# Optimization experiments

Hardware: AMD Instinct MI355X
Metric: run time of the kernel (lower is better)

## Reference

```python
import jax, jax.numpy as jnp
import numpy as np

T, B, D, H, L = 512, 64, 512, 512, 2  # seq_len, batch, input, hidden, layers (bidirectional)


def _xavier(k, shape):
    fan_out, fan_in = shape
    lim = np.sqrt(6.0 / (fan_in + fan_out)).astype(np.float32)
    return jax.random.uniform(k, shape, minval=-lim, maxval=lim, dtype=jnp.float32)


def setup_inputs() -> dict:
    key = jax.random.key(0)
    ks = jax.random.split(key, 1 + 4 * L)
    inp = {"x": jax.random.normal(ks[0], (T, B, D), dtype=jnp.float32)}
    idx = 1
    for layer in range(L):
        din = D if layer == 0 else 2 * H
        for d in ("f", "b"):
            inp[f"w_ih{layer}_{d}"] = _xavier(ks[idx], (4 * H, din)); idx += 1
            inp[f"w_hh{layer}_{d}"] = _xavier(ks[idx], (4 * H, H)); idx += 1
            # xavier_uniform() in the module fills both biases with forget_bias=1.0
            inp[f"b_ih{layer}_{d}"] = jnp.ones((4 * H,), jnp.float32)
            inp[f"b_hh{layer}_{d}"] = jnp.ones((4 * H,), jnp.float32)
    return inp


def _lstm_dir(x, w_ih, w_hh, b_ih, b_hh, reverse):
    """Run one direction of a VarLSTMCell over time. x: [T,B,Din] -> h: [T,B,H]."""
    hdim = w_hh.shape[1]
    # precompute input contribution for all timesteps (same math as per-step matmul)
    xg = jnp.einsum('tbd,gd->tbg', x, w_ih) + b_ih + b_hh  # [T,B,4H]

    def step(carry, xg_t):
        h, c = carry
        gates = xg_t + h @ w_hh.T  # [B,4H]
        i, f, g, o = jnp.split(gates, 4, axis=-1)  # PyTorch LSTMCell gate order
        c = jax.nn.sigmoid(f) * c + jax.nn.sigmoid(i) * jnp.tanh(g)
        h = jax.nn.sigmoid(o) * jnp.tanh(c)
        return (h, c), h

    init = (jnp.zeros((x.shape[1], hdim), x.dtype), jnp.zeros((x.shape[1], hdim), x.dtype))
    _, hs = jax.lax.scan(step, init, xg, reverse=reverse)
    return hs  # [T,B,H], time-ordered (scan reverse keeps original ordering)


def reference(x,
              w_ih0_f, w_hh0_f, b_ih0_f, b_hh0_f,
              w_ih0_b, w_hh0_b, b_ih0_b, b_hh0_b,
              w_ih1_f, w_hh1_f, b_ih1_f, b_hh1_f,
              w_ih1_b, w_hh1_b, b_ih1_b, b_hh1_b):
    params = [
        ((w_ih0_f, w_hh0_f, b_ih0_f, b_hh0_f), (w_ih0_b, w_hh0_b, b_ih0_b, b_hh0_b)),
        ((w_ih1_f, w_hh1_f, b_ih1_f, b_hh1_f), (w_ih1_b, w_hh1_b, b_ih1_b, b_hh1_b)),
    ]
    out = x
    for fwd_p, bwd_p in params:
        h_f = _lstm_dir(out, *fwd_p, reverse=False)
        h_b = _lstm_dir(out, *bwd_p, reverse=True)
        out = jnp.concatenate([h_f, h_b], axis=-1)  # [T,B,2H]
        # dropout=0.0 -> inter-layer dropout is identity
    return out
```

## Files before the change

kernel.cpp:

```cpp
#include <hip/hip_runtime.h>
#include <hip/hip_bf16.h>
#include <stdint.h>


typedef __attribute__((ext_vector_type(8))) _Float16 half8;
typedef __attribute__((ext_vector_type(4))) float f32x4;
typedef unsigned long long ull;

#define AL(p) __hip_atomic_load((p), __ATOMIC_RELAXED, __HIP_MEMORY_SCOPE_AGENT)
#define AS(p, v) __hip_atomic_store((p), (v), __ATOMIC_RELAXED, __HIP_MEMORY_SCOPE_AGENT)

#define TAGMASK 0x4000400040004000ULL
#define PAT_L1A 0x0000400000004000ULL
#define PAT_L1B 0x4000000040000000ULL
#define PAT_INIT_LO 0x40004000u
#define PAT_INIT_HI 0x00000000u

__device__ __forceinline__ unsigned short f2h(float f) {
    union { _Float16 h; unsigned short u; } c; c.h = (_Float16)f; return c.u;
}
__device__ __forceinline__ float h2f(unsigned short u) {
    union { _Float16 h; unsigned short u; } c; c.u = u; return (float)c.h;
}

__global__ __launch_bounds__(256) void prep_kernel(
    const float* __restrict__ x,
    const float* __restrict__ w0f, const float* __restrict__ w0b,
    const float* __restrict__ w1f, const float* __restrict__ w1b,
    const float* __restrict__ bi0f, const float* __restrict__ bh0f,
    const float* __restrict__ bi0b, const float* __restrict__ bh0b,
    const float* __restrict__ bi1f, const float* __restrict__ bh1f,
    const float* __restrict__ bi1b, const float* __restrict__ bh1b,
    unsigned short* __restrict__ xh,
    unsigned short* __restrict__ wihh,
    float* __restrict__ bias,
    uint32_t* __restrict__ hbufi)
{
    const long total = 5801984L;
    long stride = (long)gridDim.x * blockDim.x;
    for (long i = (long)blockIdx.x * blockDim.x + threadIdx.x; i < total; i += stride) {
        if (i < 4194304L) {
            float4 v = ((const float4*)x)[i];
            ushort4 o; o.x=f2h(v.x); o.y=f2h(v.y); o.z=f2h(v.z); o.w=f2h(v.w);
            ((ushort4*)xh)[i] = o;
        } else if (i < 5767168L) {
            long j = i - 4194304L;
            const float* src; long sq;
            if (j < 262144L)       { src = w0f; sq = j;            }
            else if (j < 524288L)  { src = w0b; sq = j - 262144L;  }
            else if (j < 1048576L) { src = w1f; sq = j - 524288L;  }
            else                   { src = w1b; sq = j - 1048576L; }
            float4 v = ((const float4*)src)[sq];
            ushort4 o; o.x=f2h(v.x); o.y=f2h(v.y); o.z=f2h(v.z); o.w=f2h(v.w);
            ((ushort4*)wihh)[j] = o;
        } else if (i < 5769216L) {
            long j = i - 5767168L;
            int ld = (int)(j >> 9);
            long cq = j & 511L;
            const float* bi = ld==0?bi0f: ld==1?bi0b: ld==2?bi1f:bi1b;
            const float* bh = ld==0?bh0f: ld==1?bh0b: ld==2?bh1f:bh1b;
            float4 a = ((const float4*)bi)[cq];
            float4 b = ((const float4*)bh)[cq];
            float4 o; o.x=a.x+b.x; o.y=a.y+b.y; o.z=a.z+b.z; o.w=a.w+b.w;
            ((float4*)bias)[ld*512 + cq] = o;
        } else {
            long j = i - 5769216L;
            uint4 p; p.x=PAT_INIT_LO; p.y=PAT_INIT_HI; p.z=PAT_INIT_LO; p.w=PAT_INIT_HI;
            ((uint4*)hbufi)[j] = p;
        }
    }
}

__global__ __launch_bounds__(256) void gemm_xg(
    const unsigned short* __restrict__ A,
    const unsigned short* __restrict__ Wf,
    const unsigned short* __restrict__ Wb,
    unsigned short* __restrict__ xg,
    int Din)
{
    __shared__ __align__(16) unsigned short As[4096];
    __shared__ __align__(16) unsigned short Bs[4096];
    const int dir = blockIdx.z;
    const unsigned short* W = dir ? Wb : Wf;
    unsigned short* out = xg + (size_t)dir * 32768 * 2048;
    const int bn = blockIdx.x, bm = blockIdx.y;
    const int tid = threadIdx.x;
    const int wave = tid >> 6, lane = tid & 63;
    const int q = lane >> 4, ln = lane & 15;
    const int wm = wave >> 1, wn = wave & 1;

    f32x4 acc[4][4];
#pragma unroll
    for (int a = 0; a < 4; ++a)
#pragma unroll
        for (int b = 0; b < 4; ++b) acc[a][b] = (f32x4){0.f, 0.f, 0.f, 0.f};

    const int kiter = Din >> 5;
    for (int kb = 0; kb < kiter; ++kb) {
        __syncthreads();
#pragma unroll
        for (int i = 0; i < 2; ++i) {
            int off = i*4096 + wave*1024 + lane*16;
            int row = off >> 6;
            int kel = (off & 63) >> 1;
            const unsigned short* sa = A + (size_t)(bm*128 + row)*Din + kb*32 + kel;
            const unsigned short* sb = W + (size_t)(bn*128 + row)*Din + kb*32 + kel;
            __builtin_amdgcn_global_load_lds(
                (const __attribute__((address_space(1))) uint32_t*)sa,
                (__attribute__((address_space(3))) uint32_t*)((char*)As + i*4096 + wave*1024),
                16, 0, 0);
            __builtin_amdgcn_global_load_lds(
                (const __attribute__((address_space(1))) uint32_t*)sb,
                (__attribute__((address_space(3))) uint32_t*)((char*)Bs + i*4096 + wave*1024),
                16, 0, 0);
        }
        __syncthreads();
        half8 af[4], bf[4];
#pragma unroll
        for (int mt = 0; mt < 4; ++mt)
            af[mt] = *(const half8*)((const char*)As + (wm*64 + mt*16 + ln)*64 + q*16);
#pragma unroll
        for (int nt = 0; nt < 4; ++nt)
            bf[nt] = *(const half8*)((const char*)Bs + (wn*64 + nt*16 + ln)*64 + q*16);
#pragma unroll
        for (int mt = 0; mt < 4; ++mt)
#pragma unroll
            for (int nt = 0; nt < 4; ++nt)
                acc[mt][nt] = __builtin_amdgcn_mfma_f32_16x16x32_f16(af[mt], bf[nt], acc[mt][nt], 0, 0, 0);
    }
    const int tt = bm*2 + wm;
#pragma unroll
    for (int mt = 0; mt < 4; ++mt)
#pragma unroll
        for (int nt = 0; nt < 4; ++nt) {
            int col = bn*128 + wn*64 + nt*16 + ln;
            int gate = col >> 9, colg = col & 511;
            union { unsigned short u[4]; ull v; } p;
#pragma unroll
            for (int r = 0; r < 4; ++r) p.u[r] = f2h(acc[mt][nt][r]);
            __builtin_nontemporal_store(p.v,
                (ull*)(out + (((size_t)tt*4 + gate)*512 + colg)*64 + mt*16 + q*4));
        }
}

__global__ __launch_bounds__(64) void rec_kernel(
    const unsigned short* __restrict__ xg,
    const float* __restrict__ whhf,
    const float* __restrict__ whhb,
    const float* __restrict__ bias,
    unsigned short* __restrict__ hbuf,
    unsigned short* __restrict__ outh,
    float* __restrict__ outf,
    const int layer)
{
    __shared__ __align__(16) unsigned short whh[32768];
    __shared__ __align__(16) unsigned short htile[256];
    const int bx = blockIdx.x;
    const int dir = bx & 1, g = (bx >> 1) & 31, bh = bx >> 6;
    const int lane = threadIdx.x;
    const int q = lane >> 4, ln = lane & 15;
    const float* whhg = dir ? whhb : whhf;
    const ull pat0 = layer ? PAT_L1A : 0ULL;
    const ull pat1 = layer ? PAT_L1B : TAGMASK;

    {
        const int kkw = lane >> 2, qqw = lane & 3;
#pragma unroll 4
        for (int Lr = 0; Lr < 64; ++Lr) {
            int gate = Lr >> 4, r16 = Lr & 15;
            const float* src = whhg + (size_t)(gate*512 + g*16 + r16) * 512 + lane*8;
            float4 v0 = *(const float4*)src;
            float4 v1 = *(const float4*)(src + 4);
            union { unsigned short u[8]; half8 v; } p;
            p.u[0]=f2h(v0.x); p.u[1]=f2h(v0.y); p.u[2]=f2h(v0.z); p.u[3]=f2h(v0.w);
            p.u[4]=f2h(v1.x); p.u[5]=f2h(v1.y); p.u[6]=f2h(v1.z); p.u[7]=f2h(v1.w);
            *(half8*)((char*)whh + gate*16384 + kkw*1024 + qqw*256 + r16*16) = p.v;
        }
    }
    __syncthreads();

    const unsigned short* xgd = xg + (size_t)dir * 32768 * 2048;
    const float* biasd = bias + dir * 2048;
    float bv0 = biasd[0*512 + g*16 + ln];
    float bv1 = biasd[1*512 + g*16 + ln];
    float bv2 = biasd[2*512 + g*16 + ln];
    float bv3 = biasd[3*512 + g*16 + ln];

    float carr[4] = {0.f, 0.f, 0.f, 0.f};

#pragma unroll 1
    for (int s = 0; s < 512; ++s) {
        const int t = dir ? (511 - s) : s;

        ull xv64[4];
#pragma unroll
        for (int nt = 0; nt < 4; ++nt)
            xv64[nt] = __builtin_nontemporal_load(
                (const ull*)(xgd + ((size_t)(t*4 + nt)*512 + g*16 + ln)*64 + bh*16 + q*4));

        f32x4 a0 = {0,0,0,0}, a1 = {0,0,0,0}, a2 = {0,0,0,0}, a3 = {0,0,0,0};

        if (s > 0) {
            const int slot_r = (s - 1) & 3;
            const ull epat = (((s - 1) >> 2) & 1) ? pat1 : pat0;
            const ull* hb = (const ull*)(hbuf
                + ((size_t)(slot_r*2 + dir)*64 + bh*16 + ln)*512) + q*2;
            ull hv[32];
#pragma unroll
            for (int kk = 0; kk < 16; ++kk) {
                hv[2*kk]   = AL(hb + kk*8);
                hv[2*kk+1] = AL(hb + kk*8 + 1);
            }
            for (int it = 0; it < (1 << 13); ++it) {
                unsigned stale = 0;
#pragma unroll
                for (int c = 0; c < 32; ++c)
                    stale |= ((hv[c] & TAGMASK) != epat) ? (1u << c) : 0u;
                if (!stale) break;
#pragma unroll
                for (int c = 0; c < 32; ++c)
                    if (stale & (1u << c))
                        hv[c] = AL(hb + (c >> 1)*8 + (c & 1));
            }
#pragma unroll
            for (int kk = 0; kk < 16; ++kk) {
                union { ull u[2]; half8 v; } af;
                af.u[0] = hv[2*kk]   & ~TAGMASK;
                af.u[1] = hv[2*kk+1] & ~TAGMASK;
                const char* wb = (const char*)whh + kk*1024 + lane*16;
                half8 b0 = *(const half8*)(wb);
                half8 b1 = *(const half8*)(wb + 16384);
                half8 b2 = *(const half8*)(wb + 32768);
                half8 b3 = *(const half8*)(wb + 49152);
                a0 = __builtin_amdgcn_mfma_f32_16x16x32_f16(af.v, b0, a0, 0, 0, 0);
                a1 = __builtin_amdgcn_mfma_f32_16x16x32_f16(af.v, b1, a1, 0, 0, 0);
                a2 = __builtin_amdgcn_mfma_f32_16x16x32_f16(af.v, b2, a2, 0, 0, 0);
                a3 = __builtin_amdgcn_mfma_f32_16x16x32_f16(af.v, b3, a3, 0, 0, 0);
            }
        }

        unsigned short hs[4];
#pragma unroll
        for (int r = 0; r < 4; ++r) {
            float gi = a0[r] + h2f((unsigned short)(xv64[0] >> (16*r))) + bv0;
            float gf = a1[r] + h2f((unsigned short)(xv64[1] >> (16*r))) + bv1;
            float gg = a2[r] + h2f((unsigned short)(xv64[2] >> (16*r))) + bv2;
            float go = a3[r] + h2f((unsigned short)(xv64[3] >> (16*r))) + bv3;
            float si = 1.f / (1.f + __expf(-gi));
            float sf = 1.f / (1.f + __expf(-gf));
            float so = 1.f / (1.f + __expf(-go));
            float tg = 2.f / (1.f + __expf(-2.f*gg)) - 1.f;
            float c  = sf * carr[r] + si * tg;
            carr[r] = c;
            float th = 2.f / (1.f + __expf(-2.f*c)) - 1.f;
            hs[r] = f2h(so * th);
        }

#pragma unroll
        for (int r = 0; r < 4; ++r) htile[(q*4 + r)*16 + ln] = hs[r];
        __syncthreads();
        ull hv64 = *(const ull*)(htile + (lane >> 2)*16 + (lane & 3)*4);
        const int row  = bh*16 + (lane >> 2);
        const int colw = g*16 + (lane & 3)*4;

        const int slot_w = s & 3;
        const ull wpat = ((s >> 2) & 1) ? pat1 : pat0;
        AS((ull*)(hbuf + ((size_t)(slot_w*2 + dir)*64 + row)*512 + colw), hv64 | wpat);

        if (layer == 0) {
            __builtin_nontemporal_store(hv64,
                (ull*)(outh + ((size_t)t*64 + row)*1024 + dir*512 + colw));
        } else {
            union { ull u; unsigned short us[4]; } pu; pu.u = hv64;
            union { ull u; float f[2]; } o0, o1;
            o0.f[0] = h2f(pu.us[0]); o0.f[1] = h2f(pu.us[1]);
            o1.f[0] = h2f(pu.us[2]); o1.f[1] = h2f(pu.us[3]);
            ull* dst = (ull*)(outf + ((size_t)t*64 + row)*1024 + dir*512 + colw);
            __builtin_nontemporal_store(o0.u, dst);
            __builtin_nontemporal_store(o1.u, dst + 1);
        }
        __syncthreads();
    }
}

extern "C" void kernel_launch(void* const* d_in, const int* in_sizes, int n_in,
                              void* d_out, int out_size, void* d_ws, size_t ws_size,
                              hipStream_t stream)
{
    (void)in_sizes; (void)n_in; (void)out_size; (void)ws_size;
    const float* x       = (const float*)d_in[0];
    const float* w_ih0_f = (const float*)d_in[1];
    const float* w_hh0_f = (const float*)d_in[2];
    const float* b_ih0_f = (const float*)d_in[3];
    const float* b_hh0_f = (const float*)d_in[4];
    const float* w_ih0_b = (const float*)d_in[5];
    const float* w_hh0_b = (const float*)d_in[6];
    const float* b_ih0_b = (const float*)d_in[7];
    const float* b_hh0_b = (const float*)d_in[8];
    const float* w_ih1_f = (const float*)d_in[9];
    const float* w_hh1_f = (const float*)d_in[10];
    const float* b_ih1_f = (const float*)d_in[11];
    const float* b_hh1_f = (const float*)d_in[12];
    const float* w_ih1_b = (const float*)d_in[13];
    const float* w_hh1_b = (const float*)d_in[14];
    const float* b_ih1_b = (const float*)d_in[15];
    const float* b_hh1_b = (const float*)d_in[16];

    char* ws = (char*)d_ws;
    unsigned short* xg    = (unsigned short*)(ws + 0);
    unsigned short* wihh  = (unsigned short*)(ws + 268435456L);
    float*          bias  = (float*)         (ws + 281018368L);
    unsigned short* hbuf  = (unsigned short*)(ws + 281051136L);

    unsigned short* in1 = (unsigned short*)d_out;
    unsigned short* xh  = (unsigned short*)((char*)d_out + 67108864L);
    float* outf = (float*)d_out;

    prep_kernel<<<dim3(1024), dim3(256), 0, stream>>>(
        x, w_ih0_f, w_ih0_b, w_ih1_f, w_ih1_b,
        b_ih0_f, b_hh0_f, b_ih0_b, b_hh0_b,
        b_ih1_f, b_hh1_f, b_ih1_b, b_hh1_b,
        xh, wihh, bias, (uint32_t*)hbuf);

    gemm_xg<<<dim3(16, 256, 2), dim3(256), 0, stream>>>(
        xh, wihh, wihh + 1048576, xg, 512);
    rec_kernel<<<dim3(256), dim3(64), 0, stream>>>(
        xg, w_hh0_f, w_hh0_b, bias, hbuf, in1, (float*)nullptr, 0);

    gemm_xg<<<dim3(16, 256, 2), dim3(256), 0, stream>>>(
        in1, wihh + 2097152, wihh + 4194304, xg, 1024);
    rec_kernel<<<dim3(256), dim3(64), 0, stream>>>(
        xg, w_hh1_f, w_hh1_b, bias + 4096, hbuf,
        (unsigned short*)nullptr, outf, 1);
}
```

Before: 6.215 ms.

## Restructure recurrent kernel: 8-wave blocks, register-resident weights, cooperative h staging

The recurrent kernel moves from 256 single-wave blocks to 128 blocks of 512 threads. Each wave now holds its slice of W_hh in registers instead of LDS and computes one gate for 16 columns. The block loads the previous hidden tile cooperatively with cache-bypassing dwordx4 loads and spin-checks tag bits, then stages it in swizzled LDS. Partial gate sums are exchanged through LDS, and only two waves run the nonlinearity and write h. This cuts redundant per-wave polling of the global h buffer and the LDS weight traffic, at the cost of extra block barriers per step and fewer blocks.

```diff
diff --git a/kernel.cpp b/kernel.cpp
--- a/kernel.cpp
+++ b/kernel.cpp
@@ -5,12 +5,13 @@
 
 typedef __attribute__((ext_vector_type(8))) _Float16 half8;
 typedef __attribute__((ext_vector_type(4))) float f32x4;
+typedef __attribute__((ext_vector_type(4))) uint32_t u32x4;
 typedef unsigned long long ull;
 
-#define AL(p) __hip_atomic_load((p), __ATOMIC_RELAXED, __HIP_MEMORY_SCOPE_AGENT)
 #define AS(p, v) __hip_atomic_store((p), (v), __ATOMIC_RELAXED, __HIP_MEMORY_SCOPE_AGENT)
 
 #define TAGMASK 0x4000400040004000ULL
+#define TM32    0x40004000u
 #define PAT_L1A 0x0000400000004000ULL
 #define PAT_L1B 0x4000000040000000ULL
 #define PAT_INIT_LO 0x40004000u
@@ -143,7 +144,7 @@
         }
 }
 
-__global__ __launch_bounds__(64) void rec_kernel(
+__global__ __launch_bounds__(512, 2) void rec_kernel(
     const unsigned short* __restrict__ xg,
     const float* __restrict__ whhf,
     const float* __restrict__ whhb,
@@ -153,133 +154,153 @@
     float* __restrict__ outf,
     const int layer)
 {
-    __shared__ __align__(16) unsigned short whh[32768];
-    __shared__ __align__(16) unsigned short htile[256];
+    __shared__ __align__(16) unsigned short h_lds[8192];
+    __shared__ __align__(16) float accbuf[2048];
+    __shared__ __align__(16) unsigned short htile[512];
+
     const int bx = blockIdx.x;
-    const int dir = bx & 1, g = (bx >> 1) & 31, bh = bx >> 6;
-    const int lane = threadIdx.x;
-    const int q = lane >> 4, ln = lane & 15;
+    const int dir = bx & 1, bh = (bx >> 1) & 3, cg = bx >> 3;
+    const int R0 = bh * 16, C0 = cg * 32;
+    const int tid = threadIdx.x;
+    const int wv = tid >> 6, lane = tid & 63;
+    const int g = wv >> 1, wc = wv & 1;
+    const int ln = lane & 15, q = lane >> 4;
     const float* whhg = dir ? whhb : whhf;
+
     const ull pat0 = layer ? PAT_L1A : 0ULL;
     const ull pat1 = layer ? PAT_L1B : TAGMASK;
-
+    const uint32_t ep0 = (uint32_t)(pat0 & 0xffffffffULL);
+    const uint32_t ep1 = (uint32_t)(pat1 & 0xffffffffULL);
+
+    half8 wreg[16];
     {
-        const int kkw = lane >> 2, qqw = lane & 3;
-#pragma unroll 4
-        for (int Lr = 0; Lr < 64; ++Lr) {
-            int gate = Lr >> 4, r16 = Lr & 15;
-            const float* src = whhg + (size_t)(gate*512 + g*16 + r16) * 512 + lane*8;
-            float4 v0 = *(const float4*)src;
-            float4 v1 = *(const float4*)(src + 4);
+        const int wrow = g*512 + C0 + wc*16 + ln;
+        const float* wsrc = whhg + (size_t)wrow * 512 + q*8;
+#pragma unroll
+        for (int kk = 0; kk < 16; ++kk) {
+            float4 v0 = *(const float4*)(wsrc + kk*32);
+            float4 v1 = *(const float4*)(wsrc + kk*32 + 4);
             union { unsigned short u[8]; half8 v; } p;
             p.u[0]=f2h(v0.x); p.u[1]=f2h(v0.y); p.u[2]=f2h(v0.z); p.u[3]=f2h(v0.w);
             p.u[4]=f2h(v1.x); p.u[5]=f2h(v1.y); p.u[6]=f2h(v1.z); p.u[7]=f2h(v1.w);
-            *(half8*)((char*)whh + gate*16384 + kkw*1024 + qqw*256 + r16*16) = p.v;
+            wreg[kk] = p.v;
         }
     }
-    __syncthreads();
 
     const unsigned short* xgd = xg + (size_t)dir * 32768 * 2048;
     const float* biasd = bias + dir * 2048;
-    float bv0 = biasd[0*512 + g*16 + ln];
-    float bv1 = biasd[1*512 + g*16 + ln];
-    float bv2 = biasd[2*512 + g*16 + ln];
-    float bv3 = biasd[3*512 + g*16 + ln];
-
+    const int myc = C0 + wc*16 + ln;
+    float bv0 = biasd[0*512 + myc];
+    float bv1 = biasd[1*512 + myc];
+    float bv2 = biasd[2*512 + myc];
+    float bv3 = biasd[3*512 + myc];
     float carr[4] = {0.f, 0.f, 0.f, 0.f};
+
+    const int prow = tid >> 5;
+    const int pcol = (tid & 31) * 16;
+    const int swz  = (prow & 7) << 4;
+    const int wb0 = prow*1024 + ((pcol*2)      ^ swz);
+    const int wb1 = prow*1024 + ((pcol*2 + 16) ^ swz);
 
 #pragma unroll 1
     for (int s = 0; s < 512; ++s) {
         const int t = dir ? (511 - s) : s;
 
-        ull xv64[4];
-#pragma unroll
-        for (int nt = 0; nt < 4; ++nt)
-            xv64[nt] = __builtin_nontemporal_load(
-                (const ull*)(xgd + ((size_t)(t*4 + nt)*512 + g*16 + ln)*64 + bh*16 + q*4));
-
-        f32x4 a0 = {0,0,0,0}, a1 = {0,0,0,0}, a2 = {0,0,0,0}, a3 = {0,0,0,0};
+        ull xv64[4] = {0,0,0,0};
+        if (g == 0) {
+#pragma unroll
+            for (int nt_ = 0; nt_ < 4; ++nt_)
+                xv64[nt_] = __builtin_nontemporal_load(
+                    (const ull*)(xgd + ((size_t)(t*4 + nt_)*512 + myc)*64 + bh*16 + q*4));
+        }
 
         if (s > 0) {
             const int slot_r = (s - 1) & 3;
-            const ull epat = (((s - 1) >> 2) & 1) ? pat1 : pat0;
-            const ull* hb = (const ull*)(hbuf
-                + ((size_t)(slot_r*2 + dir)*64 + bh*16 + ln)*512) + q*2;
-            ull hv[32];
+            const uint32_t ep = (((s - 1) >> 2) & 1) ? ep1 : ep0;
+            const uint32_t* src = (const uint32_t*)(hbuf
+                + ((size_t)(slot_r*2 + dir)*64 + R0 + prow)*512 + pcol);
+            u32x4 r0, r1;
+            bool ok = false;
+            for (int it = 0; it < (1 << 13) && !ok; ++it) {
+                asm volatile(
+                    "global_load_dwordx4 %0, %2, off sc0 sc1\n\t"
+                    "global_load_dwordx4 %1, %3, off sc0 sc1\n\t"
+                    "s_waitcnt vmcnt(0)"
+                    : "=&v"(r0), "=&v"(r1)
+                    : "v"(src), "v"(src + 4)
+                    : "memory");
+                uint32_t bad = 0;
+#pragma unroll
+                for (int c = 0; c < 4; ++c) bad |= (r0[c] ^ ep) & TM32;
+#pragma unroll
+                for (int c = 0; c < 4; ++c) bad |= (r1[c] ^ ep) & TM32;
+                ok = (bad == 0);
+            }
+#pragma unroll
+            for (int c = 0; c < 4; ++c) { r0[c] &= ~TM32; r1[c] &= ~TM32; }
+            *(u32x4*)((char*)h_lds + wb0) = r0;
+            *(u32x4*)((char*)h_lds + wb1) = r1;
+        }
+        __syncthreads();
+
+        f32x4 acc = (f32x4){0.f, 0.f, 0.f, 0.f};
+        if (s > 0) {
+            const char* hbase = (const char*)h_lds + ln*1024;
+            const int lswz = (ln & 7) << 4;
 #pragma unroll
             for (int kk = 0; kk < 16; ++kk) {
-                hv[2*kk]   = AL(hb + kk*8);
-                hv[2*kk+1] = AL(hb + kk*8 + 1);
+                half8 a = *(const half8*)(hbase + ((kk*64 + q*16) ^ lswz));
+                acc = __builtin_amdgcn_mfma_f32_16x16x32_f16(a, wreg[kk], acc, 0, 0, 0);
             }
-            for (int it = 0; it < (1 << 13); ++it) {
-                unsigned stale = 0;
-#pragma unroll
-                for (int c = 0; c < 32; ++c)
-                    stale |= ((hv[c] & TAGMASK) != epat) ? (1u << c) : 0u;
-                if (!stale) break;
-#pragma unroll
-                for (int c = 0; c < 32; ++c)
-                    if (stale & (1u << c))
-                        hv[c] = AL(hb + (c >> 1)*8 + (c & 1));
+        }
+        *(f32x4*)&accbuf[(wv*16 + ln)*16 + q*4] = acc;
+        __syncthreads();
+
+        if (g == 0) {
+            f32x4 a0 = *(const f32x4*)&accbuf[((0*2 + wc)*16 + ln)*16 + q*4];
+            f32x4 a1 = *(const f32x4*)&accbuf[((1*2 + wc)*16 + ln)*16 + q*4];
+            f32x4 a2 = *(const f32x4*)&accbuf[((2*2 + wc)*16 + ln)*16 + q*4];
+            f32x4 a3 = *(const f32x4*)&accbuf[((3*2 + wc)*16 + ln)*16 + q*4];
+            unsigned short hs[4];
+#pragma unroll
+            for (int r = 0; r < 4; ++r) {
+                float gi = a0[r] + h2f((unsigned short)(xv64[0] >> (16*r))) + bv0;
+                float gf = a1[r] + h2f((unsigned short)(xv64[1] >> (16*r))) + bv1;
+                float gg = a2[r] + h2f((unsigned short)(xv64[2] >> (16*r))) + bv2;
+                float go = a3[r] + h2f((unsigned short)(xv64[3] >> (16*r))) + bv3;
+                float si = 1.f / (1.f + __expf(-gi));
+                float sf = 1.f / (1.f + __expf(-gf));
+                float so = 1.f / (1.f + __expf(-go));
+                float tg = 2.f / (1.f + __expf(-2.f*gg)) - 1.f;
+                float c  = sf * carr[r] + si * tg;
+                carr[r] = c;
+                float th = 2.f / (1.f + __expf(-2.f*c)) - 1.f;
+                hs[r] = f2h(so * th);
             }
-#pragma unroll
-            for (int kk = 0; kk < 16; ++kk) {
-                union { ull u[2]; half8 v; } af;
-                af.u[0] = hv[2*kk]   & ~TAGMASK;
-                af.u[1] = hv[2*kk+1] & ~TAGMASK;
-                const char* wb = (const char*)whh + kk*1024 + lane*16;
-                half8 b0 = *(const half8*)(wb);
-                half8 b1 = *(const half8*)(wb + 16384);
-                half8 b2 = *(const half8*)(wb + 32768);
-                half8 b3 = *(const half8*)(wb + 49152);
-                a0 = __builtin_amdgcn_mfma_f32_16x16x32_f16(af.v, b0, a0, 0, 0, 0);
-                a1 = __builtin_amdgcn_mfma_f32_16x16x32_f16(af.v, b1, a1, 0, 0, 0);
-                a2 = __builtin_amdgcn_mfma_f32_16x16x32_f16(af.v, b2, a2, 0, 0, 0);
-                a3 = __builtin_amdgcn_mfma_f32_16x16x32_f16(af.v, b3, a3, 0, 0, 0);
+            unsigned short* ht = htile + wc*256;
+#pragma unroll
+            for (int r = 0; r < 4; ++r) ht[(q*4 + r)*16 + ln] = hs[r];
+            ull hv64 = *(const ull*)(ht + (lane >> 2)*16 + (lane & 3)*4);
+            const int row  = R0 + (lane >> 2);
+            const int colw = C0 + wc*16 + (lane & 3)*4;
+
+            const int slot_w = s & 3;
+            const ull wpat = ((s >> 2) & 1) ? pat1 : pat0;
+            AS((ull*)(hbuf + ((size_t)(slot_w*2 + dir)*64 + row)*512 + colw), hv64 | wpat);
+
+            if (layer == 0) {
+                __builtin_nontemporal_store(hv64,
+                    (ull*)(outh + ((size_t)t*64 + row)*1024 + dir*512 + colw));
+            } else {
+                union { ull u; unsigned short us[4]; } pu; pu.u = hv64;
+                union { ull u; float f[2]; } o0, o1;
+                o0.f[0] = h2f(pu.us[0]); o0.f[1] = h2f(pu.us[1]);
+                o1.f[0] = h2f(pu.us[2]); o1.f[1] = h2f(pu.us[3]);
+                ull* dst = (ull*)(outf + ((size_t)t*64 + row)*1024 + dir*512 + colw);
+                __builtin_nontemporal_store(o0.u, dst);
+                __builtin_nontemporal_store(o1.u, dst + 1);
             }
         }
-
-        unsigned short hs[4];
-#pragma unroll
-        for (int r = 0; r < 4; ++r) {
-            float gi = a0[r] + h2f((unsigned short)(xv64[0] >> (16*r))) + bv0;
-            float gf = a1[r] + h2f((unsigned short)(xv64[1] >> (16*r))) + bv1;
-            float gg = a2[r] + h2f((unsigned short)(xv64[2] >> (16*r))) + bv2;
-            float go = a3[r] + h2f((unsigned short)(xv64[3] >> (16*r))) + bv3;
-            float si = 1.f / (1.f + __expf(-gi));
-            float sf = 1.f / (1.f + __expf(-gf));
-            float so = 1.f / (1.f + __expf(-go));
-            float tg = 2.f / (1.f + __expf(-2.f*gg)) - 1.f;
-            float c  = sf * carr[r] + si * tg;
-            carr[r] = c;
-            float th = 2.f / (1.f + __expf(-2.f*c)) - 1.f;
-            hs[r] = f2h(so * th);
-        }
-
-#pragma unroll
-        for (int r = 0; r < 4; ++r) htile[(q*4 + r)*16 + ln] = hs[r];
-        __syncthreads();
-        ull hv64 = *(const ull*)(htile + (lane >> 2)*16 + (lane & 3)*4);
-        const int row  = bh*16 + (lane >> 2);
-        const int colw = g*16 + (lane & 3)*4;
-
-        const int slot_w = s & 3;
-        const ull wpat = ((s >> 2) & 1) ? pat1 : pat0;
-        AS((ull*)(hbuf + ((size_t)(slot_w*2 + dir)*64 + row)*512 + colw), hv64 | wpat);
-
-        if (layer == 0) {
-            __builtin_nontemporal_store(hv64,
-                (ull*)(outh + ((size_t)t*64 + row)*1024 + dir*512 + colw));
-        } else {
-            union { ull u; unsigned short us[4]; } pu; pu.u = hv64;
-            union { ull u; float f[2]; } o0, o1;
-            o0.f[0] = h2f(pu.us[0]); o0.f[1] = h2f(pu.us[1]);
-            o1.f[0] = h2f(pu.us[2]); o1.f[1] = h2f(pu.us[3]);
-            ull* dst = (ull*)(outf + ((size_t)t*64 + row)*1024 + dir*512 + colw);
-            __builtin_nontemporal_store(o0.u, dst);
-            __builtin_nontemporal_store(o1.u, dst + 1);
-        }
-        __syncthreads();
     }
 }
 
@@ -324,12 +345,12 @@
 
     gemm_xg<<<dim3(16, 256, 2), dim3(256), 0, stream>>>(
         xh, wihh, wihh + 1048576, xg, 512);
-    rec_kernel<<<dim3(256), dim3(64), 0, stream>>>(
+    rec_kernel<<<dim3(128), dim3(512), 0, stream>>>(
         xg, w_hh0_f, w_hh0_b, bias, hbuf, in1, (float*)nullptr, 0);
 
     gemm_xg<<<dim3(16, 256, 2), dim3(256), 0, stream>>>(
         in1, wihh + 2097152, wihh + 4194304, xg, 1024);
-    rec_kernel<<<dim3(256), dim3(64), 0, stream>>>(
+    rec_kernel<<<dim3(128), dim3(512), 0, stream>>>(
         xg, w_hh1_f, w_hh1_b, bias + 4096, hbuf,
         (unsigned short*)nullptr, outf, 1);
 }
```

Result: faster. 5.589 ms (-10.1%).

## Interleave both directions per block with register-resident weights and pipelined h loads

Applied to the files above, without the earlier changes.

Restructures the recurrent kernel so each 64-thread block handles both forward and backward directions for 4 hidden columns across all four gates. W_hh slices are held in registers instead of LDS, and the h ring is read with inline-asm dwordx4 coherent loads. Loads for one direction are issued while the other direction computes, hiding the cross-block polling latency. Gate values are regrouped with lane shuffles instead of an LDS tile and barriers, and each lane publishes a single tagged fp16 value. The grid doubles to 512 blocks with launch_bounds(64,2). The trade-offs are heavy register pressure, hand-written vmcnt waits that must match the exact count of loads in flight, and a new per-element tag scheme that must stay consistent with the hbuf initialisation.

```diff
diff --git a/kernel.cpp b/kernel.cpp
--- a/kernel.cpp
+++ b/kernel.cpp
@@ -5,14 +5,11 @@
 
 typedef __attribute__((ext_vector_type(8))) _Float16 half8;
 typedef __attribute__((ext_vector_type(4))) float f32x4;
+typedef __attribute__((ext_vector_type(4))) uint32_t u32x4;
 typedef unsigned long long ull;
 
-#define AL(p) __hip_atomic_load((p), __ATOMIC_RELAXED, __HIP_MEMORY_SCOPE_AGENT)
-#define AS(p, v) __hip_atomic_store((p), (v), __ATOMIC_RELAXED, __HIP_MEMORY_SCOPE_AGENT)
-
-#define TAGMASK 0x4000400040004000ULL
-#define PAT_L1A 0x0000400000004000ULL
-#define PAT_L1B 0x4000000040000000ULL
+#define TM32    0x40004000u
+#define TAGU16  ((unsigned short)0x4000)
 #define PAT_INIT_LO 0x40004000u
 #define PAT_INIT_HI 0x00000000u
 
@@ -143,7 +140,31 @@
         }
 }
 
-__global__ __launch_bounds__(64) void rec_kernel(
+#define LDQ(d, b, o) \
+    asm volatile("global_load_dwordx4 %0, %1, off offset:" o " sc0 sc1" \
+                 : "=v"(d) : "v"(b) : "memory");
+
+#define ISSUE16(hq, base) \
+    LDQ(hq[0],  base, "0")   LDQ(hq[1],  base, "64")  LDQ(hq[2],  base, "128") \
+    LDQ(hq[3],  base, "192") LDQ(hq[4],  base, "256") LDQ(hq[5],  base, "320") \
+    LDQ(hq[6],  base, "384") LDQ(hq[7],  base, "448") LDQ(hq[8],  base, "512") \
+    LDQ(hq[9],  base, "576") LDQ(hq[10], base, "640") LDQ(hq[11], base, "704") \
+    LDQ(hq[12], base, "768") LDQ(hq[13], base, "832") LDQ(hq[14], base, "896") \
+    LDQ(hq[15], base, "960")
+
+#define RETRY16(hq, base, bm) \
+    if (bm & 0x0001u) LDQ(hq[0],  base, "0")   if (bm & 0x0002u) LDQ(hq[1],  base, "64") \
+    if (bm & 0x0004u) LDQ(hq[2],  base, "128") if (bm & 0x0008u) LDQ(hq[3],  base, "192") \
+    if (bm & 0x0010u) LDQ(hq[4],  base, "256") if (bm & 0x0020u) LDQ(hq[5],  base, "320") \
+    if (bm & 0x0040u) LDQ(hq[6],  base, "384") if (bm & 0x0080u) LDQ(hq[7],  base, "448") \
+    if (bm & 0x0100u) LDQ(hq[8],  base, "512") if (bm & 0x0200u) LDQ(hq[9],  base, "576") \
+    if (bm & 0x0400u) LDQ(hq[10], base, "640") if (bm & 0x0800u) LDQ(hq[11], base, "704") \
+    if (bm & 0x1000u) LDQ(hq[12], base, "768") if (bm & 0x2000u) LDQ(hq[13], base, "832") \
+    if (bm & 0x4000u) LDQ(hq[14], base, "896") if (bm & 0x8000u) LDQ(hq[15], base, "960")
+
+#define TB(qq, ep) ((((qq)[0]^(ep)) | ((qq)[1]^(ep)) | ((qq)[2]^(ep)) | ((qq)[3]^(ep))) & TM32)
+
+__global__ __launch_bounds__(64, 2) void rec_kernel(
     const unsigned short* __restrict__ xg,
     const float* __restrict__ whhf,
     const float* __restrict__ whhb,
@@ -153,133 +174,166 @@
     float* __restrict__ outf,
     const int layer)
 {
-    __shared__ __align__(16) unsigned short whh[32768];
-    __shared__ __align__(16) unsigned short htile[256];
     const int bx = blockIdx.x;
-    const int dir = bx & 1, g = (bx >> 1) & 31, bh = bx >> 6;
+    const int bh = bx & 3, cg = bx >> 2;
+    const int R0 = bh*16, C0 = cg*4;
     const int lane = threadIdx.x;
-    const int q = lane >> 4, ln = lane & 15;
-    const float* whhg = dir ? whhb : whhf;
-    const ull pat0 = layer ? PAT_L1A : 0ULL;
-    const ull pat1 = layer ? PAT_L1B : TAGMASK;
-
+    const int ln = lane & 15, q = lane >> 4;
+    const int gate = ln & 3, lc = ln >> 2;
+    const int colg = C0 + lc;
+
+    const uint32_t ep0 = layer ? 0x00004000u : 0u;
+    const uint32_t ep1 = layer ? 0x40000000u : TM32;
+    const unsigned short wt0 = layer ? ((colg & 1) ? (unsigned short)0 : TAGU16)
+                                     : (unsigned short)0;
+    const unsigned short wt1 = layer ? ((colg & 1) ? TAGU16 : (unsigned short)0)
+                                     : TAGU16;
+
+    half8 wregA[16], wregB[16];
     {
-        const int kkw = lane >> 2, qqw = lane & 3;
-#pragma unroll 4
-        for (int Lr = 0; Lr < 64; ++Lr) {
-            int gate = Lr >> 4, r16 = Lr & 15;
-            const float* src = whhg + (size_t)(gate*512 + g*16 + r16) * 512 + lane*8;
-            float4 v0 = *(const float4*)src;
-            float4 v1 = *(const float4*)(src + 4);
+        const float* srcA = whhf + (size_t)(gate*512 + colg)*512 + q*8;
+        const float* srcB = whhb + (size_t)(gate*512 + colg)*512 + q*8;
+#pragma unroll
+        for (int kk = 0; kk < 16; ++kk) {
+            float4 v0 = *(const float4*)(srcA + kk*32);
+            float4 v1 = *(const float4*)(srcA + kk*32 + 4);
             union { unsigned short u[8]; half8 v; } p;
             p.u[0]=f2h(v0.x); p.u[1]=f2h(v0.y); p.u[2]=f2h(v0.z); p.u[3]=f2h(v0.w);
             p.u[4]=f2h(v1.x); p.u[5]=f2h(v1.y); p.u[6]=f2h(v1.z); p.u[7]=f2h(v1.w);
-            *(half8*)((char*)whh + gate*16384 + kkw*1024 + qqw*256 + r16*16) = p.v;
-        }
-    }
-    __syncthreads();
-
-    const unsigned short* xgd = xg + (size_t)dir * 32768 * 2048;
-    const float* biasd = bias + dir * 2048;
-    float bv0 = biasd[0*512 + g*16 + ln];
-    float bv1 = biasd[1*512 + g*16 + ln];
-    float bv2 = biasd[2*512 + g*16 + ln];
-    float bv3 = biasd[3*512 + g*16 + ln];
-
-    float carr[4] = {0.f, 0.f, 0.f, 0.f};
+            wregA[kk] = p.v;
+        }
+#pragma unroll
+        for (int kk = 0; kk < 16; ++kk) {
+            float4 v0 = *(const float4*)(srcB + kk*32);
+            float4 v1 = *(const float4*)(srcB + kk*32 + 4);
+            union { unsigned short u[8]; half8 v; } p;
+            p.u[0]=f2h(v0.x); p.u[1]=f2h(v0.y); p.u[2]=f2h(v0.z); p.u[3]=f2h(v0.w);
+            p.u[4]=f2h(v1.x); p.u[5]=f2h(v1.y); p.u[6]=f2h(v1.z); p.u[7]=f2h(v1.w);
+            wregB[kk] = p.v;
+        }
+    }
+
+    const unsigned short* xgdA = xg;
+    const unsigned short* xgdB = xg + (size_t)32768 * 2048;
+    const float bvA = bias[gate*512 + colg];
+    const float bvB = bias[2048 + gate*512 + colg];
+    float carrA[4] = {0.f,0.f,0.f,0.f}, carrB[4] = {0.f,0.f,0.f,0.f};
+
+    #define RINGBASE(d, sm1) ((const uint32_t*)((const char*)hbuf \
+        + ((size_t)(((sm1) & 3)*2 + (d))*64 + R0 + ln)*1024 + q*16))
+    #define XGA(t) ((const ull*)(xgdA + ((size_t)((t)*4 + gate)*512 + colg)*64 + bh*16 + q*4))
+    #define XGB(t) ((const ull*)(xgdB + ((size_t)((t)*4 + gate)*512 + colg)*64 + bh*16 + q*4))
+
+    u32x4 hqA[16], hqB[16];
+    ull xvA, xvB, xvAn, xvBn;
+
+#define PW(accv, xv, carr, bv, d, s, t) {                                         \
+        unsigned short hs[4];                                                     \
+_Pragma("unroll")                                                                 \
+        for (int r = 0; r < 4; ++r) {                                             \
+            float v  = (accv)[r] + h2f((unsigned short)((xv) >> (16*r))) + (bv);  \
+            float o1 = __shfl_xor(v, 1);                                          \
+            float e  = (gate & 1) ? o1 : v;                                       \
+            float od = (gate & 1) ? v  : o1;                                      \
+            float e2 = __shfl_xor(e, 2);                                          \
+            float od2= __shfl_xor(od, 2);                                         \
+            float gi = (gate & 2) ? e2 : e;                                       \
+            float gg = (gate & 2) ? e  : e2;                                      \
+            float gf = (gate & 2) ? od2: od;                                      \
+            float go = (gate & 2) ? od : od2;                                     \
+            float si = 1.f / (1.f + __expf(-gi));                                 \
+            float sf = 1.f / (1.f + __expf(-gf));                                 \
+            float so = 1.f / (1.f + __expf(-go));                                 \
+            float tg = 2.f / (1.f + __expf(-2.f*gg)) - 1.f;                       \
+            float c  = sf * (carr)[r] + si * tg;                                  \
+            (carr)[r] = c;                                                        \
+            float th = 2.f / (1.f + __expf(-2.f*c)) - 1.f;                        \
+            hs[r] = f2h(so * th);                                                 \
+        }                                                                         \
+        const int row = R0 + q*4 + gate;                                          \
+        unsigned short hv = hs[gate];                                             \
+        unsigned short tg16 = hv | ((((s) >> 2) & 1) ? wt1 : wt0);                \
+        __hip_atomic_store(hbuf + ((size_t)(((s) & 3)*2 + (d))*64 + row)*512 + colg, \
+                           tg16, __ATOMIC_RELAXED, __HIP_MEMORY_SCOPE_AGENT);     \
+        if (layer == 0) {                                                         \
+            __builtin_nontemporal_store(hv,                                       \
+                outh + ((size_t)(t)*64 + row)*1024 + (d)*512 + colg);             \
+        } else {                                                                  \
+            __builtin_nontemporal_store(h2f(hv),                                  \
+                outf + ((size_t)(t)*64 + row)*1024 + (d)*512 + colg);             \
+        }                                                                         \
+    }
+
+#define CHECKB(hq, ep, bmv) { bmv = 0u;                                           \
+_Pragma("unroll")                                                                 \
+        for (int k = 0; k < 16; ++k) bmv |= TB(hq[k], ep) ? (1u << k) : 0u; }
+
+#define RETRYLOOP(hq, base, ep, bmv) {                                            \
+        int it_ = 0;                                                              \
+        while (__builtin_expect(bmv != 0u, 0) && it_++ < 8192) {                  \
+            RETRY16(hq, base, bmv)                                                \
+            asm volatile("s_waitcnt vmcnt(0)" ::: "memory");                      \
+            __builtin_amdgcn_sched_barrier(0);                                    \
+            CHECKB(hq, ep, bmv)                                                   \
+        } }
+
+#define CLEAR16(hq) {                                                             \
+_Pragma("unroll")                                                                 \
+        for (int k = 0; k < 16; ++k) {                                            \
+            hq[k][0] &= ~TM32; hq[k][1] &= ~TM32;                                 \
+            hq[k][2] &= ~TM32; hq[k][3] &= ~TM32; } }
+
+#define MFMA16(hq, wreg, accv) {                                                  \
+        f32x4 a0_ = (f32x4){0.f,0.f,0.f,0.f}, a1_ = a0_;                          \
+_Pragma("unroll")                                                                 \
+        for (int k = 0; k < 16; k += 2) {                                         \
+            union { u32x4 u; half8 h; } t0_, t1_;                                 \
+            t0_.u = hq[k]; t1_.u = hq[k+1];                                       \
+            a0_ = __builtin_amdgcn_mfma_f32_16x16x32_f16(t0_.h, wreg[k],   a0_, 0, 0, 0); \
+            a1_ = __builtin_amdgcn_mfma_f32_16x16x32_f16(t1_.h, wreg[k+1], a1_, 0, 0, 0); \
+        }                                                                         \
+        accv = a0_ + a1_; }
+
+    {
+        xvA = __builtin_nontemporal_load(XGA(0));
+        xvB = __builtin_nontemporal_load(XGB(511));
+        f32x4 z = (f32x4){0.f,0.f,0.f,0.f};
+        PW(z, xvA, carrA, bvA, 0, 0, 0)
+        PW(z, xvB, carrB, bvB, 1, 0, 511)
+        xvA = __builtin_nontemporal_load(XGA(1));
+        xvB = __builtin_nontemporal_load(XGB(510));
+        const uint32_t* baseA = RINGBASE(0, 0);
+        ISSUE16(hqA, baseA)
+    }
 
 #pragma unroll 1
-    for (int s = 0; s < 512; ++s) {
-        const int t = dir ? (511 - s) : s;
-
-        ull xv64[4];
-#pragma unroll
-        for (int nt = 0; nt < 4; ++nt)
-            xv64[nt] = __builtin_nontemporal_load(
-                (const ull*)(xgd + ((size_t)(t*4 + nt)*512 + g*16 + ln)*64 + bh*16 + q*4));
-
-        f32x4 a0 = {0,0,0,0}, a1 = {0,0,0,0}, a2 = {0,0,0,0}, a3 = {0,0,0,0};
-
-        if (s > 0) {
-            const int slot_r = (s - 1) & 3;
-            const ull epat = (((s - 1) >> 2) & 1) ? pat1 : pat0;
-            const ull* hb = (const ull*)(hbuf
-                + ((size_t)(slot_r*2 + dir)*64 + bh*16 + ln)*512) + q*2;
-            ull hv[32];
-#pragma unroll
-            for (int kk = 0; kk < 16; ++kk) {
-                hv[2*kk]   = AL(hb + kk*8);
-                hv[2*kk+1] = AL(hb + kk*8 + 1);
-            }
-            for (int it = 0; it < (1 << 13); ++it) {
-                unsigned stale = 0;
-#pragma unroll
-                for (int c = 0; c < 32; ++c)
-                    stale |= ((hv[c] & TAGMASK) != epat) ? (1u << c) : 0u;
-                if (!stale) break;
-#pragma unroll
-                for (int c = 0; c < 32; ++c)
-                    if (stale & (1u << c))
-                        hv[c] = AL(hb + (c >> 1)*8 + (c & 1));
-            }
-#pragma unroll
-            for (int kk = 0; kk < 16; ++kk) {
-                union { ull u[2]; half8 v; } af;
-                af.u[0] = hv[2*kk]   & ~TAGMASK;
-                af.u[1] = hv[2*kk+1] & ~TAGMASK;
-                const char* wb = (const char*)whh + kk*1024 + lane*16;
-                half8 b0 = *(const half8*)(wb);
-                half8 b1 = *(const half8*)(wb + 16384);
-                half8 b2 = *(const half8*)(wb + 32768);
-                half8 b3 = *(const half8*)(wb + 49152);
-                a0 = __builtin_amdgcn_mfma_f32_16x16x32_f16(af.v, b0, a0, 0, 0, 0);
-                a1 = __builtin_amdgcn_mfma_f32_16x16x32_f16(af.v, b1, a1, 0, 0, 0);
-                a2 = __builtin_amdgcn_mfma_f32_16x16x32_f16(af.v, b2, a2, 0, 0, 0);
-                a3 = __builtin_amdgcn_mfma_f32_16x16x32_f16(af.v, b3, a3, 0, 0, 0);
-            }
-        }
-
-        unsigned short hs[4];
-#pragma unroll
-        for (int r = 0; r < 4; ++r) {
-            float gi = a0[r] + h2f((unsigned short)(xv64[0] >> (16*r))) + bv0;
-            float gf = a1[r] + h2f((unsigned short)(xv64[1] >> (16*r))) + bv1;
-            float gg = a2[r] + h2f((unsigned short)(xv64[2] >> (16*r))) + bv2;
-            float go = a3[r] + h2f((unsigned short)(xv64[3] >> (16*r))) + bv3;
-            float si = 1.f / (1.f + __expf(-gi));
-            float sf = 1.f / (1.f + __expf(-gf));
-            float so = 1.f / (1.f + __expf(-go));
-            float tg = 2.f / (1.f + __expf(-2.f*gg)) - 1.f;
-            float c  = sf * carr[r] + si * tg;
-            carr[r] = c;
-            float th = 2.f / (1.f + __expf(-2.f*c)) - 1.f;
-            hs[r] = f2h(so * th);
-        }
-
-#pragma unroll
-        for (int r = 0; r < 4; ++r) htile[(q*4 + r)*16 + ln] = hs[r];
-        __syncthreads();
-        ull hv64 = *(const ull*)(htile + (lane >> 2)*16 + (lane & 3)*4);
-        const int row  = bh*16 + (lane >> 2);
-        const int colw = g*16 + (lane & 3)*4;
-
-        const int slot_w = s & 3;
-        const ull wpat = ((s >> 2) & 1) ? pat1 : pat0;
-        AS((ull*)(hbuf + ((size_t)(slot_w*2 + dir)*64 + row)*512 + colw), hv64 | wpat);
-
-        if (layer == 0) {
-            __builtin_nontemporal_store(hv64,
-                (ull*)(outh + ((size_t)t*64 + row)*1024 + dir*512 + colw));
-        } else {
-            union { ull u; unsigned short us[4]; } pu; pu.u = hv64;
-            union { ull u; float f[2]; } o0, o1;
-            o0.f[0] = h2f(pu.us[0]); o0.f[1] = h2f(pu.us[1]);
-            o1.f[0] = h2f(pu.us[2]); o1.f[1] = h2f(pu.us[3]);
-            ull* dst = (ull*)(outf + ((size_t)t*64 + row)*1024 + dir*512 + colw);
-            __builtin_nontemporal_store(o0.u, dst);
-            __builtin_nontemporal_store(o1.u, dst + 1);
-        }
-        __syncthreads();
+    for (int s = 1; s < 512; ++s) {
+        const uint32_t ep = (((s - 1) >> 2) & 1) ? ep1 : ep0;
+        const uint32_t* baseA = RINGBASE(0, s - 1);
+        const uint32_t* baseB = RINGBASE(1, s - 1);
+        uint32_t bm;
+
+        asm volatile("s_waitcnt vmcnt(4)" ::: "memory");
+        __builtin_amdgcn_sched_barrier(0);
+        CHECKB(hqA, ep, bm)
+        RETRYLOOP(hqA, baseA, ep, bm)
+        CLEAR16(hqA)
+        f32x4 accA; MFMA16(hqA, wregA, accA)
+        ISSUE16(hqB, baseB)
+        PW(accA, xvA, carrA, bvA, 0, s, s)
+        if (s < 511) { const uint32_t* baseA2 = RINGBASE(0, s); ISSUE16(hqA, baseA2) }
+        asm volatile("s_waitcnt vmcnt(18)" ::: "memory");
+        __builtin_amdgcn_sched_barrier(0);
+        CHECKB(hqB, ep, bm)
+        RETRYLOOP(hqB, baseB, ep, bm)
+        CLEAR16(hqB)
+        f32x4 accB; MFMA16(hqB, wregB, accB)
+        PW(accB, xvB, carrB, bvB, 1, s, 511 - s)
+        if (s < 511) {
+            xvAn = __builtin_nontemporal_load(XGA(s + 1));
+            xvBn = __builtin_nontemporal_load(XGB(510 - s));
+            xvA = xvAn; xvB = xvBn;
+        }
     }
 }
 
@@ -324,12 +378,12 @@
 
     gemm_xg<<<dim3(16, 256, 2), dim3(256), 0, stream>>>(
         xh, wihh, wihh + 1048576, xg, 512);
-    rec_kernel<<<dim3(256), dim3(64), 0, stream>>>(
+    rec_kernel<<<dim3(512), dim3(64), 0, stream>>>(
         xg, w_hh0_f, w_hh0_b, bias, hbuf, in1, (float*)nullptr, 0);
 
     gemm_xg<<<dim3(16, 256, 2), dim3(256), 0, stream>>>(
         in1, wihh + 2097152, wihh + 4194304, xg, 1024);
-    rec_kernel<<<dim3(256), dim3(64), 0, stream>>>(
+    rec_kernel<<<dim3(512), dim3(64), 0, stream>>>(
         xg, w_hh1_f, w_hh1_b, bias + 4096, hbuf,
         (unsigned short*)nullptr, outf, 1);
 }
```

New measurement: 11.94 ms. 92.1% more time.
